# Kernel optimization log

Hardware: AMD Instinct MI355X
Metric: run time of the kernel (lower is better)

## Reference

```python
import jax, jax.numpy as jnp
import numpy as np

B, K, S, HS = 32, 8, 512, 256


def setup_inputs() -> dict:
    key = jax.random.key(0)
    ks = jax.random.split(key, 12)
    sc = 1.0 / np.sqrt(HS)
    return {
        "rem_fea": jax.random.normal(ks[0], (B, S, HS), jnp.float32),
        "ret_fea": jax.random.normal(ks[1], (B, K, S, HS), jnp.float32),
        "Wr": jax.random.normal(ks[2], (HS, HS), jnp.float32) * sc,
        "br": jax.random.normal(ks[3], (HS,), jnp.float32) * sc,
        "Wt": jax.random.normal(ks[4], (HS, HS), jnp.float32) * sc,
        "bt": jax.random.normal(ks[5], (HS,), jnp.float32) * sc,
        "W1": jax.random.normal(ks[6], (K, HS, HS), jnp.float32) * sc,
        "b1": jax.random.normal(ks[7], (K, HS), jnp.float32) * sc,
        "W2": jax.random.normal(ks[8], (K, HS, HS), jnp.float32) * sc,
        "b2": jax.random.normal(ks[9], (K, HS), jnp.float32) * sc,
    }


def reference(rem_fea, ret_fea, Wr, br, Wt, bt, W1, b1, W2, b2):
    # ---- MACRouter ----
    rem_lin = rem_fea @ Wr + br                       # [B,S,hs]
    ret_lin = jnp.einsum("bksd,de->bkse", ret_fea, Wt) + bt  # [B,K,S,hs]
    avg_rem = rem_lin.mean(axis=1)                    # [B,hs]
    avg_ret = ret_lin.mean(axis=2)                    # [B,K,hs]
    scores = jnp.einsum("bd,bkd->bk", avg_rem, avg_ret)
    routing = jax.nn.softmax(scores, axis=1)          # [B,K]
    # ---- K dense experts (batched over K) ----
    h = jax.nn.relu(jnp.einsum("bksd,kde->bkse", ret_fea, W1) + b1[None, :, None, :])
    expert_outs = jnp.einsum("bksd,kde->bkse", h, W2) + b2[None, :, None, :]
    # ---- weighted sum over experts ----
    gen_fea = jnp.einsum("bksd,bk->bsd", expert_outs, routing)
    return gen_fea
```

## Files before the change

kernel.cpp:

```cpp
#include <hip/hip_runtime.h>
#include <hip/hip_bf16.h>

typedef __attribute__((ext_vector_type(8))) short bf16x8;
typedef __attribute__((ext_vector_type(4))) float f32x4;

constexpr int Bb = 32, Kk = 8, Ss = 512, HS = 256;
constexpr int SUB = 32;
constexpr int NST = Ss / SUB;
constexpr int SUB_BYTES = SUB * HS * 2;
constexpr int MT = 64;

__device__ __forceinline__ unsigned short f2bf(float f) {
  unsigned int u = __builtin_bit_cast(unsigned int, f);
  u = (u + 0x7FFFu + ((u >> 16) & 1u)) >> 16;
  return (unsigned short)u;
}

__device__ __forceinline__ void gload_lds16(const void* g, void* l) {
  __builtin_amdgcn_global_load_lds((const __attribute__((address_space(1))) void*)g,
                                   (__attribute__((address_space(3))) void*)l, 16, 0, 0);
}

__global__ void prep(const float* __restrict__ rem, const float* __restrict__ ret,
                     const float* __restrict__ W1, const float* __restrict__ W2,
                     unsigned short* __restrict__ W1p, unsigned short* __restrict__ W2p,
                     char* __restrict__ swz, float* __restrict__ partial_ret,
                     float* __restrict__ partial_rem) {
  int blk = blockIdx.x, t = threadIdx.x;
  if (blk < 512) {
    const float* W = (blk < 256) ? W1 : W2;
    unsigned short* Wp = (blk < 256) ? W1p : W2p;
    int idx = (blk & 255) * 256 + t;
    int lane = idx & 63, nt = (idx >> 6) & 15, kk = (idx >> 10) & 7, k = idx >> 13;
    const float* src = W + ((size_t)k * HS + kk * 32 + ((lane >> 4) * 8)) * HS + nt * 16 + (lane & 15);
    unsigned short* dst = Wp + (size_t)idx * 8;
#pragma unroll
    for (int i = 0; i < 8; ++i) dst[i] = f2bf(src[(size_t)i * HS]);
    return;
  }
  blk -= 512;
  const float* src;
  float* pdst;
  char* dst = nullptr;
  if (blk < Bb * Kk * NST) {
    int st = blk & 15, bk = blk >> 4;
    src = ret + ((size_t)bk * Ss + st * SUB) * HS;
    pdst = partial_ret + (size_t)blk * HS;
    if (swz) dst = swz + (size_t)blk * SUB_BYTES;
  } else {
    int rid = blk - Bb * Kk * NST;
    int st = rid & 15, b = rid >> 4;
    src = rem + ((size_t)b * Ss + st * SUB) * HS;
    pdst = partial_rem + (size_t)rid * HS;
  }
  f32x4 acc = {0.f, 0.f, 0.f, 0.f};
#pragma unroll
  for (int j = 0; j < 8; ++j) {
    int f = j * 256 + t;
    int row = f >> 6, c4 = f & 63;
    f32x4 v = *reinterpret_cast<const f32x4*>(src + (size_t)row * HS + c4 * 4);
    acc += v;
    if (dst) {
      union { unsigned short h[4]; unsigned long long u; } pk;
      pk.h[0] = f2bf(v[0]); pk.h[1] = f2bf(v[1]); pk.h[2] = f2bf(v[2]); pk.h[3] = f2bf(v[3]);
      int off = (c4 >> 5) * 8192 + row * 256 + ((((c4 & 31) >> 1) ^ (row & 7)) * 16) + (c4 & 1) * 8;
      *reinterpret_cast<unsigned long long*>(dst + off) = pk.u;
    }
  }
  __shared__ f32x4 red[256];
  red[t] = acc;
  __syncthreads();
  if (t < 64) {
    f32x4 s = red[t] + red[t + 64] + red[t + 128] + red[t + 192];
    *reinterpret_cast<f32x4*>(pdst + t * 4) = s;
  }
}

__global__ void routing_kernel(const float* __restrict__ partial_ret, const float* __restrict__ partial_rem,
                               const float* __restrict__ Wr, const float* __restrict__ br,
                               const float* __restrict__ Wt, const float* __restrict__ bt,
                               float* __restrict__ routing) {
  int b = blockIdx.x, t = threadIdx.x;
  __shared__ float srem[HS];
  __shared__ float sret[Kk][HS];
  {
    float s = 0.f;
    for (int st = 0; st < NST; ++st) s += partial_rem[((size_t)(b * NST + st)) * HS + t];
    srem[t] = s;
    for (int k = 0; k < Kk; ++k) {
      float sk = 0.f;
      for (int st = 0; st < NST; ++st) sk += partial_ret[((size_t)((b * Kk + k) * NST + st)) * HS + t];
      sret[k][t] = sk;
    }
  }
  __syncthreads();
  float rl = 0.f;
  for (int e = 0; e < HS; ++e) rl += srem[e] * Wr[(size_t)e * HS + t];
  rl = rl * (1.f / Ss) + br[t];
  float tl[Kk];
#pragma unroll
  for (int k = 0; k < Kk; ++k) tl[k] = 0.f;
  for (int e = 0; e < HS; ++e) {
    float w = Wt[(size_t)e * HS + t];
#pragma unroll
    for (int k = 0; k < Kk; ++k) tl[k] += sret[k][e] * w;
  }
  __shared__ float sh[4];
  __shared__ float scores[Kk];
  for (int k = 0; k < Kk; ++k) {
    float p = rl * (tl[k] * (1.f / Ss) + bt[t]);
#pragma unroll
    for (int off = 32; off; off >>= 1) p += __shfl_down(p, off);
    if ((t & 63) == 0) sh[t >> 6] = p;
    __syncthreads();
    if (t == 0) scores[k] = sh[0] + sh[1] + sh[2] + sh[3];
    __syncthreads();
  }
  if (t == 0) {
    float mx = scores[0];
    for (int k = 1; k < Kk; ++k) mx = fmaxf(mx, scores[k]);
    float s = 0.f, ev[Kk];
    for (int k = 0; k < Kk; ++k) { ev[k] = expf(scores[k] - mx); s += ev[k]; }
    for (int k = 0; k < Kk; ++k) routing[b * Kk + k] = ev[k] / s;
  }
}

template <int SRC>
__launch_bounds__(512, 1)
__global__ void experts_kernel(const float* __restrict__ ret, const char* __restrict__ ret_swz,
                               const unsigned short* __restrict__ W1p,
                               const unsigned short* __restrict__ W2p,
                               const float* __restrict__ b1, const float* __restrict__ b2,
                               const float* __restrict__ routing, float* __restrict__ out) {
  __shared__ __align__(16) char A_lds[2][2 * SUB_BYTES];
  __shared__ __align__(16) char H_lds[MT * HS * 2];
  const int blk = blockIdx.x;
  const int b = blk >> 3, st64 = blk & 7;
  const int tid = threadIdx.x;
  const int wave = tid >> 6, lane = tid & 63;
  const int l15 = lane & 15, l4 = lane >> 4;

  auto stage = [&](int k, int bufi) {
    if constexpr (SRC == 0) {
      const char* tb = ret_swz + ((size_t)((b * Kk + k) * NST + st64 * 2)) * SUB_BYTES;
#pragma unroll
      for (int i = 0; i < 4; ++i) {
        int c = wave + i * 8;
        gload_lds16(tb + c * 1024 + (size_t)lane * 16, A_lds[bufi] + c * 1024);
      }
    } else {
      const float* src = ret + ((size_t)(b * Kk + k) * Ss + st64 * MT) * HS;
#pragma unroll
      for (int j = 0; j < 8; ++j) {
        int f = j * 512 + tid;
        int row = f >> 6, c4 = f & 63;
        f32x4 v = *reinterpret_cast<const f32x4*>(src + (size_t)row * HS + c4 * 4);
        union { unsigned short h[4]; unsigned long long u; } pk;
        pk.h[0] = f2bf(v[0]); pk.h[1] = f2bf(v[1]); pk.h[2] = f2bf(v[2]); pk.h[3] = f2bf(v[3]);
        int off = (row >> 5) * 16384 + (c4 >> 5) * 8192 + (row & 31) * 256 +
                  ((((c4 & 31) >> 1) ^ (row & 7)) * 16) + (c4 & 1) * 8;
        *reinterpret_cast<unsigned long long*>(A_lds[bufi] + off) = pk.u;
      }
    }
  };

  float out_acc[4][2][4];
#pragma unroll
  for (int m = 0; m < 4; ++m)
#pragma unroll
    for (int n = 0; n < 2; ++n)
#pragma unroll
      for (int i = 0; i < 4; ++i) out_acc[m][n][i] = 0.f;
  const f32x4 zero4 = {0.f, 0.f, 0.f, 0.f};

  stage(0, 0);
  __syncthreads();

  int buf = 0;
  for (int k = 0; k < Kk; ++k) {
    if (k + 1 < Kk) stage(k + 1, buf ^ 1);

    f32x4 accH[2][4];
#pragma unroll
    for (int m = 0; m < 2; ++m)
#pragma unroll
      for (int n = 0; n < 4; ++n) accH[m][n] = zero4;

    const unsigned short* W1k = W1p + (size_t)k * 65536;
#pragma unroll
    for (int kk = 0; kk < 8; ++kk) {
      bf16x8 aW[2], aA[4];
#pragma unroll
      for (int m = 0; m < 2; ++m)
        aW[m] = *reinterpret_cast<const bf16x8*>(W1k + ((size_t)(kk * 16 + wave * 2 + m) * 64 + lane) * 8);
#pragma unroll
      for (int n = 0; n < 4; ++n) {
        int srow = n * 16 + l15;
        int r5 = srow & 31;
        int off = (srow >> 5) * 16384 + (kk >> 2) * 8192 + r5 * 256 +
                  ((((kk & 3) * 4 + l4) ^ (r5 & 7)) * 16);
        aA[n] = *reinterpret_cast<const bf16x8*>(A_lds[buf] + off);
      }
#pragma unroll
      for (int m = 0; m < 2; ++m)
#pragma unroll
        for (int n = 0; n < 4; ++n)
          accH[m][n] = __builtin_amdgcn_mfma_f32_16x16x32_bf16(aW[m], aA[n], accH[m][n], 0, 0, 0);
    }

#pragma unroll
    for (int m = 0; m < 2; ++m) {
      int e0 = wave * 32 + m * 16 + l4 * 4;
      float4 b1v = *reinterpret_cast<const float4*>(b1 + k * HS + e0);
#pragma unroll
      for (int n = 0; n < 4; ++n) {
        int srow = n * 16 + l15;
        union { unsigned short h[4]; unsigned long long u; } pk;
        pk.h[0] = f2bf(fmaxf(accH[m][n][0] + b1v.x, 0.f));
        pk.h[1] = f2bf(fmaxf(accH[m][n][1] + b1v.y, 0.f));
        pk.h[2] = f2bf(fmaxf(accH[m][n][2] + b1v.z, 0.f));
        pk.h[3] = f2bf(fmaxf(accH[m][n][3] + b1v.w, 0.f));
        int boff = srow * 512 + ((e0 * 2) ^ ((srow & 7) << 4));
        *reinterpret_cast<unsigned long long*>(H_lds + boff) = pk.u;
      }
    }
    asm volatile("s_waitcnt lgkmcnt(0)\n\ts_barrier" ::: "memory");

    f32x4 acc2[4][2];
#pragma unroll
    for (int m = 0; m < 4; ++m)
#pragma unroll
      for (int n = 0; n < 2; ++n) acc2[m][n] = zero4;

    const unsigned short* W2k = W2p + (size_t)k * 65536;
#pragma unroll
    for (int kk = 0; kk < 8; ++kk) {
      bf16x8 aH[4], bW[2];
#pragma unroll
      for (int m = 0; m < 4; ++m) {
        int r = m * 16 + l15;
        int boff = r * 512 + ((kk * 64 + l4 * 16) ^ ((r & 7) << 4));
        aH[m] = *reinterpret_cast<const bf16x8*>(H_lds + boff);
      }
#pragma unroll
      for (int n = 0; n < 2; ++n)
        bW[n] = *reinterpret_cast<const bf16x8*>(W2k + ((size_t)(kk * 16 + wave * 2 + n) * 64 + lane) * 8);
#pragma unroll
      for (int m = 0; m < 4; ++m)
#pragma unroll
        for (int n = 0; n < 2; ++n)
          acc2[m][n] = __builtin_amdgcn_mfma_f32_16x16x32_bf16(aH[m], bW[n], acc2[m][n], 0, 0, 0);
    }

    float rw = routing[b * Kk + k];
#pragma unroll
    for (int n = 0; n < 2; ++n) {
      int col = (wave * 2 + n) * 16 + l15;
      float b2v = b2[k * HS + col];
#pragma unroll
      for (int m = 0; m < 4; ++m)
#pragma unroll
        for (int i = 0; i < 4; ++i) out_acc[m][n][i] += rw * (acc2[m][n][i] + b2v);
    }
    asm volatile("s_waitcnt vmcnt(0) lgkmcnt(0)\n\ts_barrier" ::: "memory");
    buf ^= 1;
  }

#pragma unroll
  for (int m = 0; m < 4; ++m)
#pragma unroll
    for (int i = 0; i < 4; ++i) {
      int row = m * 16 + l4 * 4 + i;
      float* orow = out + ((size_t)b * Ss + st64 * MT + row) * HS;
#pragma unroll
      for (int n = 0; n < 2; ++n) orow[(wave * 2 + n) * 16 + l15] = out_acc[m][n][i];
    }
}

extern "C" void kernel_launch(void* const* d_in, const int* in_sizes, int n_in,
                              void* d_out, int out_size, void* d_ws, size_t ws_size,
                              hipStream_t stream) {
  const float* rem = (const float*)d_in[0];
  const float* ret = (const float*)d_in[1];
  const float* Wr  = (const float*)d_in[2];
  const float* br  = (const float*)d_in[3];
  const float* Wt  = (const float*)d_in[4];
  const float* bt  = (const float*)d_in[5];
  const float* W1  = (const float*)d_in[6];
  const float* b1  = (const float*)d_in[7];
  const float* W2  = (const float*)d_in[8];
  const float* b2  = (const float*)d_in[9];
  float* out = (float*)d_out;

  char* w = (char*)d_ws;
  unsigned short* W1p = (unsigned short*)w;
  unsigned short* W2p = (unsigned short*)(w + (1u << 20));
  float* partial_ret  = (float*)(w + (2u << 20));
  float* partial_rem  = (float*)(w + (6u << 20));
  float* routing      = (float*)(w + (6u << 20) + (512u << 10));
  char*  ret_swz      = w + (7u << 20);

  bool full = ws_size >= ((size_t)71 << 20);

  prep<<<512 + Bb * Kk * NST + Bb * NST, 256, 0, stream>>>(rem, ret, W1, W2, W1p, W2p,
                                                           full ? ret_swz : nullptr,
                                                           partial_ret, partial_rem);
  routing_kernel<<<Bb, 256, 0, stream>>>(partial_ret, partial_rem, Wr, br, Wt, bt, routing);
  if (full)
    experts_kernel<0><<<Bb * (Ss / MT), 512, 0, stream>>>(ret, ret_swz, W1p, W2p, b1, b2, routing, out);
  else
    experts_kernel<1><<<Bb * (Ss / MT), 512, 0, stream>>>(ret, nullptr, W1p, W2p, b1, b2, routing, out);
}
```

Measured before the change: 117.2 us.

## Software-pipeline expert GEMMs with double-buffered hidden activations in LDS

Double-buffers the hidden-activation tile in LDS so that the second GEMM of expert k-1 runs in the same loop step as the first GEMM and ReLU epilogue of expert k. This drops the mid-iteration barrier, leaving one barrier per expert instead of two. It also gives the scheduler two independent MFMA streams to interleave. The cost is another 32 KB of LDS, more live accumulator registers, and a peeled prologue and epilogue.

```diff
diff --git a/kernel.cpp b/kernel.cpp
--- a/kernel.cpp
+++ b/kernel.cpp
@@ -133,7 +133,7 @@
                                const float* __restrict__ b1, const float* __restrict__ b2,
                                const float* __restrict__ routing, float* __restrict__ out) {
   __shared__ __align__(16) char A_lds[2][2 * SUB_BYTES];
-  __shared__ __align__(16) char H_lds[MT * HS * 2];
+  __shared__ __align__(16) char H_lds[2][MT * HS * 2];
   const int blk = blockIdx.x;
   const int b = blk >> 3, st64 = blk & 7;
   const int tid = threadIdx.x;
@@ -164,28 +164,7 @@
     }
   };
 
-  float out_acc[4][2][4];
-#pragma unroll
-  for (int m = 0; m < 4; ++m)
-#pragma unroll
-    for (int n = 0; n < 2; ++n)
-#pragma unroll
-      for (int i = 0; i < 4; ++i) out_acc[m][n][i] = 0.f;
-  const f32x4 zero4 = {0.f, 0.f, 0.f, 0.f};
-
-  stage(0, 0);
-  __syncthreads();
-
-  int buf = 0;
-  for (int k = 0; k < Kk; ++k) {
-    if (k + 1 < Kk) stage(k + 1, buf ^ 1);
-
-    f32x4 accH[2][4];
-#pragma unroll
-    for (int m = 0; m < 2; ++m)
-#pragma unroll
-      for (int n = 0; n < 4; ++n) accH[m][n] = zero4;
-
+  auto gemm1 = [&](int k, int abuf, f32x4 (&accH)[2][4]) {
     const unsigned short* W1k = W1p + (size_t)k * 65536;
 #pragma unroll
     for (int kk = 0; kk < 8; ++kk) {
@@ -199,7 +178,7 @@
         int r5 = srow & 31;
         int off = (srow >> 5) * 16384 + (kk >> 2) * 8192 + r5 * 256 +
                   ((((kk & 3) * 4 + l4) ^ (r5 & 7)) * 16);
-        aA[n] = *reinterpret_cast<const bf16x8*>(A_lds[buf] + off);
+        aA[n] = *reinterpret_cast<const bf16x8*>(A_lds[abuf] + off);
       }
 #pragma unroll
       for (int m = 0; m < 2; ++m)
@@ -207,7 +186,9 @@
         for (int n = 0; n < 4; ++n)
           accH[m][n] = __builtin_amdgcn_mfma_f32_16x16x32_bf16(aW[m], aA[n], accH[m][n], 0, 0, 0);
     }
-
+  };
+
+  auto epilogue1 = [&](int k, int hbuf, f32x4 (&accH)[2][4]) {
 #pragma unroll
     for (int m = 0; m < 2; ++m) {
       int e0 = wave * 32 + m * 16 + l4 * 4;
@@ -221,17 +202,26 @@
         pk.h[2] = f2bf(fmaxf(accH[m][n][2] + b1v.z, 0.f));
         pk.h[3] = f2bf(fmaxf(accH[m][n][3] + b1v.w, 0.f));
         int boff = srow * 512 + ((e0 * 2) ^ ((srow & 7) << 4));
-        *reinterpret_cast<unsigned long long*>(H_lds + boff) = pk.u;
-      }
-    }
-    asm volatile("s_waitcnt lgkmcnt(0)\n\ts_barrier" ::: "memory");
-
+        *reinterpret_cast<unsigned long long*>(H_lds[hbuf] + boff) = pk.u;
+      }
+    }
+  };
+
+  float out_acc[4][2][4];
+#pragma unroll
+  for (int m = 0; m < 4; ++m)
+#pragma unroll
+    for (int n = 0; n < 2; ++n)
+#pragma unroll
+      for (int i = 0; i < 4; ++i) out_acc[m][n][i] = 0.f;
+  const f32x4 zero4 = {0.f, 0.f, 0.f, 0.f};
+
+  auto gemm2_acc = [&](int k, int hbuf) {
     f32x4 acc2[4][2];
 #pragma unroll
     for (int m = 0; m < 4; ++m)
 #pragma unroll
       for (int n = 0; n < 2; ++n) acc2[m][n] = zero4;
-
     const unsigned short* W2k = W2p + (size_t)k * 65536;
 #pragma unroll
     for (int kk = 0; kk < 8; ++kk) {
@@ -240,7 +230,7 @@
       for (int m = 0; m < 4; ++m) {
         int r = m * 16 + l15;
         int boff = r * 512 + ((kk * 64 + l4 * 16) ^ ((r & 7) << 4));
-        aH[m] = *reinterpret_cast<const bf16x8*>(H_lds + boff);
+        aH[m] = *reinterpret_cast<const bf16x8*>(H_lds[hbuf] + boff);
       }
 #pragma unroll
       for (int n = 0; n < 2; ++n)
@@ -251,7 +241,6 @@
         for (int n = 0; n < 2; ++n)
           acc2[m][n] = __builtin_amdgcn_mfma_f32_16x16x32_bf16(aH[m], bW[n], acc2[m][n], 0, 0, 0);
     }
-
     float rw = routing[b * Kk + k];
 #pragma unroll
     for (int n = 0; n < 2; ++n) {
@@ -262,9 +251,37 @@
 #pragma unroll
         for (int i = 0; i < 4; ++i) out_acc[m][n][i] += rw * (acc2[m][n][i] + b2v);
     }
+  };
+
+  stage(0, 0);
+  asm volatile("s_waitcnt vmcnt(0) lgkmcnt(0)\n\ts_barrier" ::: "memory");
+
+  {
+    stage(1, 1);
+    f32x4 accH[2][4];
+#pragma unroll
+    for (int m = 0; m < 2; ++m)
+#pragma unroll
+      for (int n = 0; n < 4; ++n) accH[m][n] = zero4;
+    gemm1(0, 0, accH);
+    epilogue1(0, 0, accH);
+  }
+  asm volatile("s_waitcnt vmcnt(0) lgkmcnt(0)\n\ts_barrier" ::: "memory");
+
+  for (int p = 1; p < Kk; ++p) {
+    if (p + 1 < Kk) stage(p + 1, (p + 1) & 1);
+    gemm2_acc(p - 1, (p - 1) & 1);
+    f32x4 accH[2][4];
+#pragma unroll
+    for (int m = 0; m < 2; ++m)
+#pragma unroll
+      for (int n = 0; n < 4; ++n) accH[m][n] = zero4;
+    gemm1(p, p & 1, accH);
+    epilogue1(p, p & 1, accH);
     asm volatile("s_waitcnt vmcnt(0) lgkmcnt(0)\n\ts_barrier" ::: "memory");
-    buf ^= 1;
-  }
+  }
+
+  gemm2_acc(Kk - 1, (Kk - 1) & 1);
 
 #pragma unroll
   for (int m = 0; m < 4; ++m)
```

After: 123.1 us. 1.05x slower.

## Fold routing weight into H, accumulate experts in MFMA, single-buffer A tile

Applied to the files above, without the earlier changes.

The routing weight is now multiplied into the ReLU hidden activations before the bf16 pack, so the second GEMM accumulates straight into the shared output accumulator through the MFMA C operand, and the routed b2 bias sum is added once at the end. This removes the per-expert acc2 registers and the scalar multiply-add epilogue. The A tile is now single-buffered, and the prefetch of the next expert's input is issued after the H barrier so it overlaps the second GEMM. The aim is lower register and LDS use. The cost is a shorter overlap window for the prefetch, and the routing weight now passes through bf16 rounding before the second GEMM.

```diff
diff --git a/kernel.cpp b/kernel.cpp
--- a/kernel.cpp
+++ b/kernel.cpp
@@ -132,7 +132,7 @@
                                const unsigned short* __restrict__ W2p,
                                const float* __restrict__ b1, const float* __restrict__ b2,
                                const float* __restrict__ routing, float* __restrict__ out) {
-  __shared__ __align__(16) char A_lds[2][2 * SUB_BYTES];
+  __shared__ __align__(16) char A_lds[2 * SUB_BYTES];
   __shared__ __align__(16) char H_lds[MT * HS * 2];
   const int blk = blockIdx.x;
   const int b = blk >> 3, st64 = blk & 7;
@@ -140,13 +140,26 @@
   const int wave = tid >> 6, lane = tid & 63;
   const int l15 = lane & 15, l4 = lane >> 4;
 
-  auto stage = [&](int k, int bufi) {
+  float rw[Kk];
+#pragma unroll
+  for (int k = 0; k < Kk; ++k) rw[k] = routing[b * Kk + k];
+  float bias2[2];
+#pragma unroll
+  for (int n = 0; n < 2; ++n) {
+    int col = (wave * 2 + n) * 16 + l15;
+    float s = 0.f;
+#pragma unroll
+    for (int k = 0; k < Kk; ++k) s += rw[k] * b2[k * HS + col];
+    bias2[n] = s;
+  }
+
+  auto stage = [&](int k) {
     if constexpr (SRC == 0) {
       const char* tb = ret_swz + ((size_t)((b * Kk + k) * NST + st64 * 2)) * SUB_BYTES;
 #pragma unroll
       for (int i = 0; i < 4; ++i) {
         int c = wave + i * 8;
-        gload_lds16(tb + c * 1024 + (size_t)lane * 16, A_lds[bufi] + c * 1024);
+        gload_lds16(tb + c * 1024 + (size_t)lane * 16, A_lds + c * 1024);
       }
     } else {
       const float* src = ret + ((size_t)(b * Kk + k) * Ss + st64 * MT) * HS;
@@ -159,7 +172,7 @@
         pk.h[0] = f2bf(v[0]); pk.h[1] = f2bf(v[1]); pk.h[2] = f2bf(v[2]); pk.h[3] = f2bf(v[3]);
         int off = (row >> 5) * 16384 + (c4 >> 5) * 8192 + (row & 31) * 256 +
                   ((((c4 & 31) >> 1) ^ (row & 7)) * 16) + (c4 & 1) * 8;
-        *reinterpret_cast<unsigned long long*>(A_lds[bufi] + off) = pk.u;
+        *reinterpret_cast<unsigned long long*>(A_lds + off) = pk.u;
       }
     }
   };
@@ -173,13 +186,10 @@
       for (int i = 0; i < 4; ++i) out_acc[m][n][i] = 0.f;
   const f32x4 zero4 = {0.f, 0.f, 0.f, 0.f};
 
-  stage(0, 0);
-  __syncthreads();
-
-  int buf = 0;
+  stage(0);
+  asm volatile("s_waitcnt vmcnt(0) lgkmcnt(0)\n\ts_barrier" ::: "memory");
+
   for (int k = 0; k < Kk; ++k) {
-    if (k + 1 < Kk) stage(k + 1, buf ^ 1);
-
     f32x4 accH[2][4];
 #pragma unroll
     for (int m = 0; m < 2; ++m)
@@ -199,7 +209,7 @@
         int r5 = srow & 31;
         int off = (srow >> 5) * 16384 + (kk >> 2) * 8192 + r5 * 256 +
                   ((((kk & 3) * 4 + l4) ^ (r5 & 7)) * 16);
-        aA[n] = *reinterpret_cast<const bf16x8*>(A_lds[buf] + off);
+        aA[n] = *reinterpret_cast<const bf16x8*>(A_lds + off);
       }
 #pragma unroll
       for (int m = 0; m < 2; ++m)
@@ -208,29 +218,28 @@
           accH[m][n] = __builtin_amdgcn_mfma_f32_16x16x32_bf16(aW[m], aA[n], accH[m][n], 0, 0, 0);
     }
 
-#pragma unroll
-    for (int m = 0; m < 2; ++m) {
-      int e0 = wave * 32 + m * 16 + l4 * 4;
-      float4 b1v = *reinterpret_cast<const float4*>(b1 + k * HS + e0);
-#pragma unroll
-      for (int n = 0; n < 4; ++n) {
-        int srow = n * 16 + l15;
-        union { unsigned short h[4]; unsigned long long u; } pk;
-        pk.h[0] = f2bf(fmaxf(accH[m][n][0] + b1v.x, 0.f));
-        pk.h[1] = f2bf(fmaxf(accH[m][n][1] + b1v.y, 0.f));
-        pk.h[2] = f2bf(fmaxf(accH[m][n][2] + b1v.z, 0.f));
-        pk.h[3] = f2bf(fmaxf(accH[m][n][3] + b1v.w, 0.f));
-        int boff = srow * 512 + ((e0 * 2) ^ ((srow & 7) << 4));
-        *reinterpret_cast<unsigned long long*>(H_lds + boff) = pk.u;
+    {
+      float r = rw[k];
+#pragma unroll
+      for (int m = 0; m < 2; ++m) {
+        int e0 = wave * 32 + m * 16 + l4 * 4;
+        float4 b1v = *reinterpret_cast<const float4*>(b1 + k * HS + e0);
+#pragma unroll
+        for (int n = 0; n < 4; ++n) {
+          int srow = n * 16 + l15;
+          union { unsigned short h[4]; unsigned long long u; } pk;
+          pk.h[0] = f2bf(fmaxf(accH[m][n][0] + b1v.x, 0.f) * r);
+          pk.h[1] = f2bf(fmaxf(accH[m][n][1] + b1v.y, 0.f) * r);
+          pk.h[2] = f2bf(fmaxf(accH[m][n][2] + b1v.z, 0.f) * r);
+          pk.h[3] = f2bf(fmaxf(accH[m][n][3] + b1v.w, 0.f) * r);
+          int boff = srow * 512 + ((e0 * 2) ^ ((srow & 7) << 4));
+          *reinterpret_cast<unsigned long long*>(H_lds + boff) = pk.u;
+        }
       }
     }
     asm volatile("s_waitcnt lgkmcnt(0)\n\ts_barrier" ::: "memory");
 
-    f32x4 acc2[4][2];
-#pragma unroll
-    for (int m = 0; m < 4; ++m)
-#pragma unroll
-      for (int n = 0; n < 2; ++n) acc2[m][n] = zero4;
+    if (k + 1 < Kk) stage(k + 1);
 
     const unsigned short* W2k = W2p + (size_t)k * 65536;
 #pragma unroll
@@ -248,22 +257,14 @@
 #pragma unroll
       for (int m = 0; m < 4; ++m)
 #pragma unroll
-        for (int n = 0; n < 2; ++n)
-          acc2[m][n] = __builtin_amdgcn_mfma_f32_16x16x32_bf16(aH[m], bW[n], acc2[m][n], 0, 0, 0);
-    }
-
-    float rw = routing[b * Kk + k];
-#pragma unroll
-    for (int n = 0; n < 2; ++n) {
-      int col = (wave * 2 + n) * 16 + l15;
-      float b2v = b2[k * HS + col];
-#pragma unroll
-      for (int m = 0; m < 4; ++m)
-#pragma unroll
-        for (int i = 0; i < 4; ++i) out_acc[m][n][i] += rw * (acc2[m][n][i] + b2v);
+        for (int n = 0; n < 2; ++n) {
+          f32x4 c = {out_acc[m][n][0], out_acc[m][n][1], out_acc[m][n][2], out_acc[m][n][3]};
+          c = __builtin_amdgcn_mfma_f32_16x16x32_bf16(aH[m], bW[n], c, 0, 0, 0);
+          out_acc[m][n][0] = c[0]; out_acc[m][n][1] = c[1];
+          out_acc[m][n][2] = c[2]; out_acc[m][n][3] = c[3];
+        }
     }
     asm volatile("s_waitcnt vmcnt(0) lgkmcnt(0)\n\ts_barrier" ::: "memory");
-    buf ^= 1;
   }
 
 #pragma unroll
@@ -273,7 +274,8 @@
       int row = m * 16 + l4 * 4 + i;
       float* orow = out + ((size_t)b * Ss + st64 * MT + row) * HS;
 #pragma unroll
-      for (int n = 0; n < 2; ++n) orow[(wave * 2 + n) * 16 + l15] = out_acc[m][n][i];
+      for (int n = 0; n < 2; ++n)
+        orow[(wave * 2 + n) * 16 + l15] = out_acc[m][n][i] + bias2[n];
     }
 }
 
```

Result: slower. 129.2 us (+10.2%).
